# Kernel optimization log

Measured on AMD Instinct MI355X. Metric: run time of the kernel, lower is better.

Reference implementation:

```python
import jax, jax.numpy as jnp
import numpy as np

B, T, D = 32, 512, 384
DUR_MAX = 8                 # durations drawn in [0, DUR_MAX)
MAX_OUT = T * (DUR_MAX - 1) # static upper bound on total expanded length (3584)
ALPHA = 1.0


def setup_inputs() -> dict:
    key = jax.random.key(0)
    k1, k2 = jax.random.split(key)
    x = jax.random.normal(k1, (B, T, D), dtype=jnp.float32)
    durations = jax.random.randint(k2, (B, T), 0, DUR_MAX, dtype=jnp.int32)
    return {"input": x, "durations": durations}


def reference(input, durations):
    # patched_dur = clamp(round(alpha * dur), min=0)
    patched = jnp.round(ALPHA * durations.astype(jnp.float32)).astype(jnp.int32)
    patched = jnp.maximum(patched, 0)                       # [B, T]
    cum = jnp.cumsum(patched, axis=1)                       # [B, T] exclusive-right boundaries
    total = cum[:, -1:]                                      # [B, 1] true expanded lengths

    pos = jnp.arange(MAX_OUT, dtype=jnp.int32)               # [MAX_OUT]
    # output frame j comes from token idx = first t with cum[t] > j
    idx = jax.vmap(lambda c: jnp.searchsorted(c, pos, side='right'))(cum)  # [B, MAX_OUT]
    idx = jnp.clip(idx, 0, T - 1)
    valid = pos[None, :] < total                              # [B, MAX_OUT]

    out = jnp.take_along_axis(input, idx[:, :, None], axis=1)  # [B, MAX_OUT, D]
    return jnp.where(valid[:, :, None], out, jnp.zeros((), dtype=input.dtype))
```

## Files before the change

kernel.cpp:

```cpp
#include <hip/hip_runtime.h>

#define NB 32
#define NT 512
#define ND 384
#define DUR_MAX 8
#define MAX_OUT (NT * (DUR_MAX - 1))
#define NV (ND / 4)
#define NWIN 16
#define WPOS (MAX_OUT / NWIN)
#define NBLK (NB * NWIN)
#define VPT (WPOS * NV / NT)

__global__ __launch_bounds__(NT) void lr_fused(
    const int* __restrict__ dur, const float4* __restrict__ in,
    float4* __restrict__ out)
{
    __shared__ int wsum[NT / 64];
    __shared__ int ridx[WPOS];

    const unsigned bid = blockIdx.x;
    const unsigned l   = (bid & 7u) * (NBLK / 8u) + (bid >> 3);
    const int b  = (int)(l >> 4);
    const int wb = (int)(l & 15u);
    const int p0 = wb * WPOS;

    const int t    = threadIdx.x;
    const int lane = t & 63;
    const int w    = t >> 6;

    if (t < WPOS) ridx[t] = -1;

    int d = dur[b * NT + t];
    d = d > 0 ? d : 0;

    int v = d;
    #pragma unroll
    for (int off = 1; off < 64; off <<= 1) {
        int u = __shfl_up(v, off);
        if (lane >= off) v += u;
    }
    if (lane == 63) wsum[w] = v;
    __syncthreads();
    if (t == 0) {
        int acc = 0;
        #pragma unroll
        for (int i = 0; i < NT / 64; ++i) { acc += wsum[i]; wsum[i] = acc; }
    }
    __syncthreads();
    const int cum   = v + (w ? wsum[w - 1] : 0);
    const int start = cum - d;

    int lo = start - p0;        if (lo < 0) lo = 0;
    int hi = start + d - p0;    if (hi > WPOS) hi = WPOS;
    const int src = (b * NT + t) * NV;
    for (int j = lo; j < hi; ++j) ridx[j] = src;
    __syncthreads();

    float4* ob = out + ((size_t)b * MAX_OUT + p0) * NV;
    for (int i = 0; i < VPT; ++i) {
        const int g = i * NT + t;
        const int r = g / NV;
        const int c = g - r * NV;
        const int s = ridx[r];
        const int sa = s >= 0 ? s : 0;
        const float4 ld = in[sa + c];
        float4 val = make_float4(0.f, 0.f, 0.f, 0.f);
        if (s >= 0) val = ld;
        ob[g] = val;
    }
}

extern "C" void kernel_launch(void* const* d_in, const int* in_sizes, int n_in,
                              void* d_out, int out_size, void* d_ws, size_t ws_size,
                              hipStream_t stream)
{
    const float* x   = (const float*)d_in[0];
    const int*   dur = (const int*)d_in[1];
    float* out = (float*)d_out;

    lr_fused<<<NBLK, NT, 0, stream>>>(dur, (const float4*)x, (float4*)out);
}
```

Before: 203.4 us.

## Halve block size, double windows, scan two durations per thread, use nontemporal stores

The block now has 256 threads instead of 512, and each thread loads two durations as an int2 for the prefix scan. The output is split into 32 windows per batch instead of 16, which doubles the number of smaller blocks. The serial cross-wave scan done by thread 0 is replaced by each thread summing the wave totals itself. Output writes use nontemporal stores so the large write stream is not cached, and the input load is now predicated so zero rows skip the gather. This aims to improve parallelism and reduce cache pollution on a write-bound kernel, at the cost of more per-thread work in the scan and fill steps.

```diff
diff --git a/kernel.cpp b/kernel.cpp
--- a/kernel.cpp
+++ b/kernel.cpp
@@ -1,27 +1,29 @@
 #include <hip/hip_runtime.h>
 
 #define NB 32
-#define NT 512
+#define NTDUR 512
+#define NT 256
 #define ND 384
-#define DUR_MAX 8
-#define MAX_OUT (NT * (DUR_MAX - 1))
+#define MAX_OUT 3584
 #define NV (ND / 4)
-#define NWIN 16
+#define NWIN 32
 #define WPOS (MAX_OUT / NWIN)
 #define NBLK (NB * NWIN)
 #define VPT (WPOS * NV / NT)
 
+typedef float f32x4 __attribute__((ext_vector_type(4)));
+
 __global__ __launch_bounds__(NT) void lr_fused(
-    const int* __restrict__ dur, const float4* __restrict__ in,
-    float4* __restrict__ out)
+    const int* __restrict__ dur, const f32x4* __restrict__ in,
+    f32x4* __restrict__ out)
 {
     __shared__ int wsum[NT / 64];
     __shared__ int ridx[WPOS];
 
     const unsigned bid = blockIdx.x;
     const unsigned l   = (bid & 7u) * (NBLK / 8u) + (bid >> 3);
-    const int b  = (int)(l >> 4);
-    const int wb = (int)(l & 15u);
+    const int b  = (int)(l >> 5);
+    const int wb = (int)(l & 31u);
     const int p0 = wb * WPOS;
 
     const int t    = threadIdx.x;
@@ -30,10 +32,12 @@
 
     if (t < WPOS) ridx[t] = -1;
 
-    int d = dur[b * NT + t];
-    d = d > 0 ? d : 0;
+    const int2 dd = ((const int2*)dur)[b * (NTDUR / 2) + t];
+    const int d0 = dd.x > 0 ? dd.x : 0;
+    const int d1 = dd.y > 0 ? dd.y : 0;
+    const int s  = d0 + d1;
 
-    int v = d;
+    int v = s;
     #pragma unroll
     for (int off = 1; off < 64; off <<= 1) {
         int u = __shfl_up(v, off);
@@ -41,32 +45,37 @@
     }
     if (lane == 63) wsum[w] = v;
     __syncthreads();
-    if (t == 0) {
-        int acc = 0;
-        #pragma unroll
-        for (int i = 0; i < NT / 64; ++i) { acc += wsum[i]; wsum[i] = acc; }
+
+    int prev = 0;
+    #pragma unroll
+    for (int i = 0; i < NT / 64; ++i) prev += (i < w) ? wsum[i] : 0;
+    const int excl = prev + v - s;
+
+    const int row0 = b * NTDUR + 2 * t;
+    const int en0  = excl + d0;
+    {
+        int lo = excl - p0; if (lo < 0) lo = 0;
+        int hi = en0  - p0; if (hi > WPOS) hi = WPOS;
+        const int src = row0 * NV;
+        for (int j = lo; j < hi; ++j) ridx[j] = src;
+    }
+    {
+        int lo = en0 - p0;      if (lo < 0) lo = 0;
+        int hi = en0 + d1 - p0; if (hi > WPOS) hi = WPOS;
+        const int src = (row0 + 1) * NV;
+        for (int j = lo; j < hi; ++j) ridx[j] = src;
     }
     __syncthreads();
-    const int cum   = v + (w ? wsum[w - 1] : 0);
-    const int start = cum - d;
 
-    int lo = start - p0;        if (lo < 0) lo = 0;
-    int hi = start + d - p0;    if (hi > WPOS) hi = WPOS;
-    const int src = (b * NT + t) * NV;
-    for (int j = lo; j < hi; ++j) ridx[j] = src;
-    __syncthreads();
-
-    float4* ob = out + ((size_t)b * MAX_OUT + p0) * NV;
+    f32x4* ob = out + ((size_t)b * MAX_OUT + p0) * NV;
     for (int i = 0; i < VPT; ++i) {
         const int g = i * NT + t;
         const int r = g / NV;
         const int c = g - r * NV;
-        const int s = ridx[r];
-        const int sa = s >= 0 ? s : 0;
-        const float4 ld = in[sa + c];
-        float4 val = make_float4(0.f, 0.f, 0.f, 0.f);
-        if (s >= 0) val = ld;
-        ob[g] = val;
+        const int sv = ridx[r];
+        f32x4 val = (f32x4)(0.f);
+        if (sv >= 0) val = in[sv + c];
+        __builtin_nontemporal_store(val, &ob[g]);
     }
 }
 
@@ -78,5 +87,5 @@
     const int*   dur = (const int*)d_in[1];
     float* out = (float*)d_out;
 
-    lr_fused<<<NBLK, NT, 0, stream>>>(dur, (const float4*)x, (float4*)out);
+    lr_fused<<<NBLK, NT, 0, stream>>>(dur, (const f32x4*)x, (f32x4*)out);
 }
```

Measured after the change: 213.1 us. +4.8%, slower.
